# Kernel optimization log

Measured on AMD Instinct MI355X. Metric: run time of the kernel, lower is better.

Reference implementation:

```python
import jax, jax.numpy as jnp
import numpy as np
import math

B, S, E = 4, 4096, 1024
NUM_HEADS = 16
D = E // NUM_HEADS  # attention_size = 64


def setup_inputs() -> dict:
    key = jax.random.key(0)
    ks = jax.random.split(key, 7)
    queries = jax.random.normal(ks[0], (B, S, E), dtype=jnp.float32)
    keys = jax.random.normal(ks[1], (B, S, E), dtype=jnp.float32)
    values = jax.random.normal(ks[2], (B, S, E), dtype=jnp.float32)
    mask = jax.random.randint(ks[3], (B, S, S), 0, 2).astype(bool)
    # nn.Linear(E, D, bias=False): weight [D, E], y = x @ W^T
    lim = 1.0 / math.sqrt(E)
    W_q = jax.random.uniform(ks[4], (D, E), jnp.float32, -lim, lim)
    W_k = jax.random.uniform(ks[5], (D, E), jnp.float32, -lim, lim)
    W_v = jax.random.uniform(ks[6], (D, E), jnp.float32, -lim, lim)
    return {"queries": queries, "keys": keys, "values": values, "mask": mask,
            "W_q": W_q, "W_k": W_k, "W_v": W_v}


def reference(queries, keys, values, mask, W_q, W_k, W_v):
    Q = jnp.einsum('bse,de->bsd', queries, W_q)  # [B,S,D]
    K = jnp.einsum('bse,de->bsd', keys, W_k)
    V = jnp.einsum('bse,de->bsd', values, W_v)
    norm = math.sqrt(D)
    scores = jnp.einsum('bqd,bkd->bqk', Q, K) / norm  # [B,S,S]
    scores = jnp.where(mask, jnp.float32(-1e20), scores)
    attn = jax.nn.softmax(scores, axis=2)
    return jnp.einsum('bqk,bkd->bqd', attn, V)  # [B,S,D]
```

## Files before the change

kernel.cpp:

```cpp
#include <hip/hip_runtime.h>
#include <hip/hip_bf16.h>
#include <math.h>

#define NB 4
#define NS 4096
#define NE 1024
#define ND 64

typedef short bf16x8 __attribute__((ext_vector_type(8)));
typedef float f32x4  __attribute__((ext_vector_type(4)));

__device__ unsigned short g_Wb[3 * ND * NE];
__device__ unsigned short g_Qp[NB * NS * ND];
__device__ unsigned short g_Kp[NB * NS * ND];
__device__ unsigned short g_Vt[NB * ND * NS];
__device__ int g_flag;

static __device__ inline unsigned short f2bf(float f) {
    __hip_bfloat16 h = __float2bfloat16(f);
    return *reinterpret_cast<unsigned short*>(&h);
}
static __device__ inline unsigned int f2bf2(float lo, float hi) {
    __hip_bfloat162 h = __float22bfloat162_rn(make_float2(lo, hi));
    return *reinterpret_cast<unsigned int*>(&h);
}

static __device__ __forceinline__ void lds_fence() {
    asm volatile("s_waitcnt lgkmcnt(0)" ::: "memory");
}

__global__ void detect_mask(const unsigned int* __restrict__ mw) {
    __shared__ int found;
    if (threadIdx.x == 0) found = 0;
    __syncthreads();
    int f = 0;
    for (int i = threadIdx.x; i < 4096; i += 256)
        if (mw[i] > 1u) f = 1;
    if (f) atomicOr(&found, 1);
    __syncthreads();
    if (threadIdx.x == 0) g_flag = found;
}

__global__ void prep_w(const float* __restrict__ Wq, const float* __restrict__ Wk,
                       const float* __restrict__ Wv) {
    const int z = blockIdx.x;
    const float* W = (z == 0) ? Wq : (z == 1) ? Wk : Wv;
    unsigned short* o = g_Wb + (size_t)z * (ND * NE);
    const float scale = (z == 0) ? 0.125f : 1.0f;
    int i0 = blockIdx.y * 2048 + threadIdx.x * 8;
    float4 a = *(const float4*)&W[i0];
    float4 b = *(const float4*)&W[i0 + 4];
    ushort4 u0 = { f2bf(a.x * scale), f2bf(a.y * scale), f2bf(a.z * scale), f2bf(a.w * scale) };
    ushort4 u1 = { f2bf(b.x * scale), f2bf(b.y * scale), f2bf(b.z * scale), f2bf(b.w * scale) };
    *(ushort4*)&o[i0]     = u0;
    *(ushort4*)&o[i0 + 4] = u1;
}

__global__ __launch_bounds__(256) void proj_kernel(
    const float* __restrict__ Xq, const float* __restrict__ Xk, const float* __restrict__ Xv)
{
    __shared__ unsigned short Xs[2][64][72];

    const int z = blockIdx.y;
    const float* X = (z == 0) ? Xq : (z == 1) ? Xk : Xv;
    const unsigned short* W = g_Wb + (size_t)z * (ND * NE);

    const int t    = threadIdx.x;
    const int wv   = t >> 6;
    const int lane = t & 63;
    const int quad = lane >> 4;
    const int l16  = lane & 15;
    const int m0   = blockIdx.x * 64;

    const int sr  = t >> 4;
    const int sc4 = (t & 15) * 4;
    const float* Xb = X + (size_t)m0 * NE;

    float4 xr[4][4];

    #pragma unroll
    for (int d = 0; d < 4; ++d)
        #pragma unroll
        for (int p = 0; p < 4; ++p)
            xr[d][p] = *(const float4*)&Xb[(size_t)(sr + p * 16) * NE + d * 64 + sc4];
    #pragma unroll
    for (int p = 0; p < 4; ++p) {
        uint2 u = { f2bf2(xr[0][p].x, xr[0][p].y), f2bf2(xr[0][p].z, xr[0][p].w) };
        *(uint2*)&Xs[0][sr + p * 16][sc4] = u;
    }
    __syncthreads();

    f32x4 acc[4] = {};

    #pragma unroll
    for (int c = 0; c < 16; ++c) {
        if (c + 4 < 16) {
            #pragma unroll
            for (int p = 0; p < 4; ++p)
                xr[c & 3][p] = *(const float4*)&Xb[(size_t)(sr + p * 16) * NE + (c + 4) * 64 + sc4];
        }

        #pragma unroll
        for (int ks = 0; ks < 2; ++ks) {
            bf16x8 a = *(const bf16x8*)&Xs[c & 1][wv * 16 + l16][ks * 32 + quad * 8];
            #pragma unroll
            for (int nt = 0; nt < 4; ++nt) {
                bf16x8 bb = *(const bf16x8*)&W[(size_t)(nt * 16 + l16) * NE + c * 64 + ks * 32 + quad * 8];
                acc[nt] = __builtin_amdgcn_mfma_f32_16x16x32_bf16(a, bb, acc[nt], 0, 0, 0);
            }
        }

        if (c + 1 < 16) {
            #pragma unroll
            for (int p = 0; p < 4; ++p) {
                float4 v = xr[(c + 1) & 3][p];
                uint2 u = { f2bf2(v.x, v.y), f2bf2(v.z, v.w) };
                *(uint2*)&Xs[(c + 1) & 1][sr + p * 16][sc4] = u;
            }
        }
        __syncthreads();
    }

    #pragma unroll
    for (int nt = 0; nt < 4; ++nt)
        #pragma unroll
        for (int r = 0; r < 4; ++r) {
            int m   = m0 + wv * 16 + quad * 4 + r;
            int col = nt * 16 + l16;
            unsigned short u = f2bf(acc[nt][r]);
            if (z == 0)      g_Qp[(size_t)m * ND + col] = u;
            else if (z == 1) g_Kp[(size_t)m * ND + col] = u;
            else             g_Vt[((size_t)(m >> 12) * ND + col) * NS + (m & 4095)] = u;
        }
}

__global__ __launch_bounds__(256, 4) void attn_kernel(
    const void* __restrict__ maskp, float* __restrict__ out)
{
    __shared__ __align__(16) char smem[28672];
    short (*Ss)[2][16][72]         = reinterpret_cast<short(*)[2][16][72]>(smem);
    unsigned char (*Mb)[2][16][80] = reinterpret_cast<unsigned char(*)[2][16][80]>(smem + 18432);
    float (*Op)[16][68]            = reinterpret_cast<float(*)[16][68]>(smem);
    float (*Lp)[16]                = reinterpret_cast<float(*)[16]>(smem + 17408);

    const int t    = threadIdx.x;
    const int wv   = t >> 6;
    const int lane = t & 63;
    const int quad = lane >> 4;
    const int l16  = lane & 15;
    const int b    = blockIdx.y;
    const int q0   = blockIdx.x * 16;
    const int koff = wv * 1024;

    const bool m_u8 = (g_flag != 0);
    const unsigned char* m8  = (const unsigned char*)maskp;
    const int*           m32 = (const int*)maskp;

    const unsigned short* Qrow = g_Qp + ((size_t)b * NS + q0 + l16) * ND;
    const bf16x8 qf0 = *(const bf16x8*)&Qrow[quad * 8];
    const bf16x8 qf1 = *(const bf16x8*)&Qrow[32 + quad * 8];

    const unsigned short* Kbase = g_Kp + ((size_t)b * NS) * ND;
    const unsigned short* Vbase = g_Vt + (size_t)b * ND * NS;

    const int srow = lane >> 2;
    const int scol = (lane & 3) * 16;
    const unsigned char* m8row = m8 + ((size_t)b * NS + q0 + srow) * (size_t)NS + scol;

    if (m_u8) {
        uint4 mr0 = *(const uint4*)&m8row[koff];
        *(uint4*)&Mb[wv][0][srow][scol] = mr0;
    }

    float l_lane[4] = {};
    f32x4 Oacc[4] = {};

    #pragma unroll 2
    for (int it = 0; it < 16; ++it) {
        const int k0 = koff + it * 64;
        const int pb = it & 1;

        f32x4 sc[4] = {};
        #pragma unroll
        for (int kt = 0; kt < 4; ++kt) {
            const unsigned short* Krow = Kbase + (size_t)(k0 + kt * 16 + l16) * ND;
            bf16x8 kf0 = *(const bf16x8*)&Krow[quad * 8];
            bf16x8 kf1 = *(const bf16x8*)&Krow[32 + quad * 8];
            sc[kt] = __builtin_amdgcn_mfma_f32_16x16x32_bf16(qf0, kf0, sc[kt], 0, 0, 0);
            sc[kt] = __builtin_amdgcn_mfma_f32_16x16x32_bf16(qf1, kf1, sc[kt], 0, 0, 0);
        }

        uint4 mr = {};
        if (m_u8 && it < 15)
            mr = *(const uint4*)&m8row[k0 + 64];

        bf16x8 vf[8];
        #pragma unroll
        for (int nt = 0; nt < 4; ++nt) {
            const unsigned short* Vrow = Vbase + (size_t)(nt * 16 + l16) * NS + k0;
            vf[2 * nt]     = *(const bf16x8*)&Vrow[quad * 8];
            vf[2 * nt + 1] = *(const bf16x8*)&Vrow[32 + quad * 8];
        }

        int mvv[16];
        if (m_u8) {
            #pragma unroll
            for (int kt = 0; kt < 4; ++kt)
                #pragma unroll
                for (int r = 0; r < 4; ++r)
                    mvv[kt * 4 + r] = Mb[wv][pb][quad * 4 + r][kt * 16 + l16];
        } else {
            #pragma unroll
            for (int r = 0; r < 4; ++r) {
                size_t mrow = ((size_t)b * NS + (q0 + quad * 4 + r)) * (size_t)NS + k0;
                #pragma unroll
                for (int kt = 0; kt < 4; ++kt)
                    mvv[kt * 4 + r] = m32[mrow + kt * 16 + l16];
            }
        }

        #pragma unroll
        for (int kt = 0; kt < 4; ++kt)
            #pragma unroll
            for (int r = 0; r < 4; ++r) {
                float p = mvv[kt * 4 + r] ? 0.0f : __expf(sc[kt][r]);
                l_lane[r] += p;
                Ss[wv][pb][quad * 4 + r][kt * 16 + l16] = (short)f2bf(p);
            }

        if (m_u8 && it < 15)
            *(uint4*)&Mb[wv][pb ^ 1][srow][scol] = mr;

        lds_fence();

        bf16x8 a0 = *(const bf16x8*)&Ss[wv][pb][l16][quad * 8];
        bf16x8 a1 = *(const bf16x8*)&Ss[wv][pb][l16][32 + quad * 8];

        __builtin_amdgcn_s_setprio(1);
        #pragma unroll
        for (int nt = 0; nt < 4; ++nt) {
            Oacc[nt] = __builtin_amdgcn_mfma_f32_16x16x32_bf16(a0, vf[2 * nt],     Oacc[nt], 0, 0, 0);
            Oacc[nt] = __builtin_amdgcn_mfma_f32_16x16x32_bf16(a1, vf[2 * nt + 1], Oacc[nt], 0, 0, 0);
        }
        __builtin_amdgcn_s_setprio(0);
    }

    __syncthreads();

    #pragma unroll
    for (int r = 0; r < 4; ++r) {
        #pragma unroll
        for (int off = 1; off < 16; off <<= 1)
            l_lane[r] += __shfl_xor(l_lane[r], off);
    }

    #pragma unroll
    for (int nt = 0; nt < 4; ++nt)
        #pragma unroll
        for (int r = 0; r < 4; ++r)
            Op[wv][quad * 4 + r][nt * 16 + l16] = Oacc[nt][r];
    if (l16 == 0) {
        #pragma unroll
        for (int r = 0; r < 4; ++r)
            Lp[wv][quad * 4 + r] = l_lane[r];
    }
    __syncthreads();

    {
        int q  = t >> 4;
        int d4 = (t & 15) * 4;
        f32x4 s = {};
        #pragma unroll
        for (int w = 0; w < 4; ++w)
            s += *(const f32x4*)&Op[w][q][d4];
        float l = Lp[0][q] + Lp[1][q] + Lp[2][q] + Lp[3][q];
        float inv = 1.0f / l;
        float4 o = { s[0] * inv, s[1] * inv, s[2] * inv, s[3] * inv };
        *(float4*)&out[((size_t)b * NS + q0 + q) * ND + d4] = o;
    }
}

extern "C" void kernel_launch(void* const* d_in, const int* in_sizes, int n_in,
                              void* d_out, int out_size, void* d_ws, size_t ws_size,
                              hipStream_t stream) {
    const float* queries = (const float*)d_in[0];
    const float* keys    = (const float*)d_in[1];
    const float* values  = (const float*)d_in[2];
    const void*  mask    = d_in[3];
    const float* Wq      = (const float*)d_in[4];
    const float* Wk      = (const float*)d_in[5];
    const float* Wv      = (const float*)d_in[6];
    float* out = (float*)d_out;

    hipLaunchKernelGGL(detect_mask, dim3(1), dim3(256), 0, stream,
                       (const unsigned int*)mask);
    hipLaunchKernelGGL(prep_w, dim3(3, 32), dim3(256), 0, stream, Wq, Wk, Wv);
    hipLaunchKernelGGL(proj_kernel, dim3((NB * NS) / 64, 3), dim3(256), 0, stream,
                       queries, keys, values);
    hipLaunchKernelGGL(attn_kernel, dim3(NS / 16, NB), dim3(256), 0, stream,
                       mask, out);
}
```

Measured before the change: 607.2 us.

## Share K/V tiles in LDS across waves with async global-to-LDS double buffering

The attention kernel now gives each block 64 query rows (16 per wave) instead of splitting the key range across waves. K and V tiles are loaded once per block into swizzled, double-buffered LDS with global_load_lds, and the mask bytes are prefetched two tiles ahead. Masking is applied to the packed bf16 probability fragments, the row sum is taken from those fragments, and the cross-wave reduction of partial outputs is removed. Blocks are mapped so that each XCD works on a single batch for L2 locality. In exchange the kernel adds a block-wide barrier every tile and holds fewer blocks (a quarter as many).

```diff
diff --git a/kernel.cpp b/kernel.cpp
--- a/kernel.cpp
+++ b/kernel.cpp
@@ -24,9 +24,14 @@
     __hip_bfloat162 h = __float22bfloat162_rn(make_float2(lo, hi));
     return *reinterpret_cast<unsigned int*>(&h);
 }
-
-static __device__ __forceinline__ void lds_fence() {
-    asm volatile("s_waitcnt lgkmcnt(0)" ::: "memory");
+static __device__ inline float bf2f(short s) {
+    return __uint_as_float(((unsigned int)(unsigned short)s) << 16);
+}
+
+#define AS1 __attribute__((address_space(1)))
+#define AS3 __attribute__((address_space(3)))
+static __device__ __forceinline__ void gll16(const void* g, void* l) {
+    __builtin_amdgcn_global_load_lds((const AS1 void*)g, (AS3 void*)l, 16, 0, 0);
 }
 
 __global__ void detect_mask(const unsigned int* __restrict__ mw) {
@@ -134,149 +139,218 @@
         }
 }
 
-__global__ __launch_bounds__(256, 4) void attn_kernel(
+__global__ __launch_bounds__(256) void attn_kernel(
     const void* __restrict__ maskp, float* __restrict__ out)
 {
-    __shared__ __align__(16) char smem[28672];
-    short (*Ss)[2][16][72]         = reinterpret_cast<short(*)[2][16][72]>(smem);
-    unsigned char (*Mb)[2][16][80] = reinterpret_cast<unsigned char(*)[2][16][80]>(smem + 18432);
-    float (*Op)[16][68]            = reinterpret_cast<float(*)[16][68]>(smem);
-    float (*Lp)[16]                = reinterpret_cast<float(*)[16]>(smem + 17408);
+    __shared__ unsigned short KT[2][64 * 64];
+    __shared__ unsigned short VT[2][64 * 64];
+    __shared__ unsigned char  MR[4][4][1024];
+    __shared__ short          Ss[4][16][72];
 
     const int t    = threadIdx.x;
     const int wv   = t >> 6;
     const int lane = t & 63;
     const int quad = lane >> 4;
     const int l16  = lane & 15;
-    const int b    = blockIdx.y;
-    const int q0   = blockIdx.x * 16;
-    const int koff = wv * 1024;
+
+    const int n    = blockIdx.x;
+    const int xcd  = n & 7;
+    const int b    = xcd >> 1;
+    const int q0   = ((n >> 3) * 2 + (xcd & 1)) * 64;
+    const int wq0  = q0 + wv * 16;
 
     const bool m_u8 = (g_flag != 0);
     const unsigned char* m8  = (const unsigned char*)maskp;
     const int*           m32 = (const int*)maskp;
 
-    const unsigned short* Qrow = g_Qp + ((size_t)b * NS + q0 + l16) * ND;
+    const unsigned short* Qrow = g_Qp + ((size_t)b * NS + wq0 + l16) * ND;
     const bf16x8 qf0 = *(const bf16x8*)&Qrow[quad * 8];
     const bf16x8 qf1 = *(const bf16x8*)&Qrow[32 + quad * 8];
 
     const unsigned short* Kbase = g_Kp + ((size_t)b * NS) * ND;
     const unsigned short* Vbase = g_Vt + (size_t)b * ND * NS;
 
-    const int srow = lane >> 2;
-    const int scol = (lane & 3) * 16;
-    const unsigned char* m8row = m8 + ((size_t)b * NS + q0 + srow) * (size_t)NS + scol;
+    const int r8 = lane >> 3;
+    const int c8 = lane & 7;
+    const int sw = c8 ^ r8;
+
+    const unsigned char* m8base =
+        m8 + ((size_t)b * NS + wq0 + (lane >> 2)) * (size_t)NS + (lane & 3) * 16;
+
+    float l_row = 0.0f;
+    f32x4 Oacc[4] = {};
+
+    const int rsw = l16 & 7;
 
     if (m_u8) {
-        uint4 mr0 = *(const uint4*)&m8row[koff];
-        *(uint4*)&Mb[wv][0][srow][scol] = mr0;
+        #pragma unroll
+        for (int j = 0; j < 2; ++j) {
+            const int row = wv * 16 + j * 8 + r8;
+            gll16(Kbase + (size_t)row * 64 + sw * 8, &KT[0][(wv * 16 + j * 8) * 64]);
+            gll16(Vbase + (size_t)row * 4096 + sw * 8, &VT[0][(wv * 16 + j * 8) * 64]);
+        }
+        gll16(m8base, &MR[0][wv][0]);
+        gll16(m8base + 64, &MR[1][wv][0]);
+        asm volatile("s_waitcnt vmcnt(1)" ::: "memory");
+        __builtin_amdgcn_s_barrier();
+
+        #pragma unroll 2
+        for (int it = 0; it < 64; ++it) {
+            const int buf = it & 1;
+            const int k0  = it * 64;
+
+            if (it < 63) {
+                const int k1 = k0 + 64;
+                #pragma unroll
+                for (int j = 0; j < 2; ++j) {
+                    const int row = wv * 16 + j * 8 + r8;
+                    gll16(Kbase + (size_t)(k1 + row) * 64 + sw * 8,
+                          &KT[buf ^ 1][(wv * 16 + j * 8) * 64]);
+                    gll16(Vbase + (size_t)row * 4096 + k1 + sw * 8,
+                          &VT[buf ^ 1][(wv * 16 + j * 8) * 64]);
+                }
+            }
+            if (it < 62)
+                gll16(m8base + (it + 2) * 64, &MR[(it + 2) & 3][wv][0]);
+
+            f32x4 sc[4] = {};
+            #pragma unroll
+            for (int kt = 0; kt < 4; ++kt) {
+                const int row = kt * 16 + l16;
+                bf16x8 kf0 = *(const bf16x8*)&KT[buf][row * 64 + ((quad ^ rsw) << 3)];
+                bf16x8 kf1 = *(const bf16x8*)&KT[buf][row * 64 + (((4 + quad) ^ rsw) << 3)];
+                sc[kt] = __builtin_amdgcn_mfma_f32_16x16x32_bf16(qf0, kf0, sc[kt], 0, 0, 0);
+                sc[kt] = __builtin_amdgcn_mfma_f32_16x16x32_bf16(qf1, kf1, sc[kt], 0, 0, 0);
+            }
+
+            #pragma unroll
+            for (int kt = 0; kt < 4; ++kt)
+                #pragma unroll
+                for (int r = 0; r < 4; ++r)
+                    Ss[wv][quad * 4 + r][kt * 16 + l16] = (short)f2bf(__expf(sc[kt][r]));
+
+            asm volatile("s_waitcnt lgkmcnt(0)" ::: "memory");
+
+            bf16x8 a0 = *(const bf16x8*)&Ss[wv][l16][quad * 8];
+            bf16x8 a1 = *(const bf16x8*)&Ss[wv][l16][32 + quad * 8];
+            {
+                const unsigned char* MRt = &MR[it & 3][wv][0];
+                uint2 mm0 = *(const uint2*)&MRt[l16 * 64 + quad * 8];
+                uint2 mm1 = *(const uint2*)&MRt[l16 * 64 + 32 + quad * 8];
+                #pragma unroll
+                for (int j = 0; j < 4; ++j) {
+                    a0[j]     = ((mm0.x >> (8 * j)) & 255u) ? (short)0 : a0[j];
+                    a0[4 + j] = ((mm0.y >> (8 * j)) & 255u) ? (short)0 : a0[4 + j];
+                    a1[j]     = ((mm1.x >> (8 * j)) & 255u) ? (short)0 : a1[j];
+                    a1[4 + j] = ((mm1.y >> (8 * j)) & 255u) ? (short)0 : a1[4 + j];
+                }
+            }
+            {
+                float ls = 0.0f;
+                #pragma unroll
+                for (int j = 0; j < 8; ++j) ls += bf2f(a0[j]) + bf2f(a1[j]);
+                l_row += ls;
+            }
+            #pragma unroll
+            for (int nt = 0; nt < 4; ++nt) {
+                const int row = nt * 16 + l16;
+                bf16x8 vf0 = *(const bf16x8*)&VT[buf][row * 64 + ((quad ^ rsw) << 3)];
+                bf16x8 vf1 = *(const bf16x8*)&VT[buf][row * 64 + (((4 + quad) ^ rsw) << 3)];
+                Oacc[nt] = __builtin_amdgcn_mfma_f32_16x16x32_bf16(a0, vf0, Oacc[nt], 0, 0, 0);
+                Oacc[nt] = __builtin_amdgcn_mfma_f32_16x16x32_bf16(a1, vf1, Oacc[nt], 0, 0, 0);
+            }
+
+            if (it < 63) {
+                if (it < 62) asm volatile("s_waitcnt vmcnt(1)" ::: "memory");
+                else         asm volatile("s_waitcnt vmcnt(0)" ::: "memory");
+                __builtin_amdgcn_s_barrier();
+            }
+        }
+    } else {
+        #pragma unroll
+        for (int j = 0; j < 2; ++j) {
+            const int row = wv * 16 + j * 8 + r8;
+            gll16(Kbase + (size_t)row * 64 + sw * 8, &KT[0][(wv * 16 + j * 8) * 64]);
+            gll16(Vbase + (size_t)row * 4096 + sw * 8, &VT[0][(wv * 16 + j * 8) * 64]);
+        }
+        asm volatile("s_waitcnt vmcnt(0)" ::: "memory");
+        __builtin_amdgcn_s_barrier();
+
+        #pragma unroll 2
+        for (int it = 0; it < 64; ++it) {
+            const int buf = it & 1;
+            const int k0  = it * 64;
+
+            if (it < 63) {
+                const int k1 = k0 + 64;
+                #pragma unroll
+                for (int j = 0; j < 2; ++j) {
+                    const int row = wv * 16 + j * 8 + r8;
+                    gll16(Kbase + (size_t)(k1 + row) * 64 + sw * 8,
+                          &KT[buf ^ 1][(wv * 16 + j * 8) * 64]);
+                    gll16(Vbase + (size_t)row * 4096 + k1 + sw * 8,
+                          &VT[buf ^ 1][(wv * 16 + j * 8) * 64]);
+                }
+            }
+
+            f32x4 sc[4] = {};
+            #pragma unroll
+            for (int kt = 0; kt < 4; ++kt) {
+                const int row = kt * 16 + l16;
+                bf16x8 kf0 = *(const bf16x8*)&KT[buf][row * 64 + ((quad ^ rsw) << 3)];
+                bf16x8 kf1 = *(const bf16x8*)&KT[buf][row * 64 + (((4 + quad) ^ rsw) << 3)];
+                sc[kt] = __builtin_amdgcn_mfma_f32_16x16x32_bf16(qf0, kf0, sc[kt], 0, 0, 0);
+                sc[kt] = __builtin_amdgcn_mfma_f32_16x16x32_bf16(qf1, kf1, sc[kt], 0, 0, 0);
+            }
+
+            #pragma unroll
+            for (int r = 0; r < 4; ++r) {
+                size_t mrow = ((size_t)b * NS + (wq0 + quad * 4 + r)) * (size_t)NS + k0;
+                #pragma unroll
+                for (int kt = 0; kt < 4; ++kt) {
+                    int mv = m32[mrow + kt * 16 + l16];
+                    float p = mv ? 0.0f : __expf(sc[kt][r]);
+                    Ss[wv][quad * 4 + r][kt * 16 + l16] = (short)f2bf(p);
+                }
+            }
+
+            asm volatile("s_waitcnt lgkmcnt(0)" ::: "memory");
+
+            bf16x8 a0 = *(const bf16x8*)&Ss[wv][l16][quad * 8];
+            bf16x8 a1 = *(const bf16x8*)&Ss[wv][l16][32 + quad * 8];
+            {
+                float ls = 0.0f;
+                #pragma unroll
+                for (int j = 0; j < 8; ++j) ls += bf2f(a0[j]) + bf2f(a1[j]);
+                l_row += ls;
+            }
+            #pragma unroll
+            for (int nt = 0; nt < 4; ++nt) {
+                const int row = nt * 16 + l16;
+                bf16x8 vf0 = *(const bf16x8*)&VT[buf][row * 64 + ((quad ^ rsw) << 3)];
+                bf16x8 vf1 = *(const bf16x8*)&VT[buf][row * 64 + (((4 + quad) ^ rsw) << 3)];
+                Oacc[nt] = __builtin_amdgcn_mfma_f32_16x16x32_bf16(a0, vf0, Oacc[nt], 0, 0, 0);
+                Oacc[nt] = __builtin_amdgcn_mfma_f32_16x16x32_bf16(a1, vf1, Oacc[nt], 0, 0, 0);
+            }
+
+            if (it < 63) {
+                asm volatile("s_waitcnt vmcnt(0)" ::: "memory");
+                __builtin_amdgcn_s_barrier();
+            }
+        }
     }
 
-    float l_lane[4] = {};
-    f32x4 Oacc[4] = {};
-
-    #pragma unroll 2
-    for (int it = 0; it < 16; ++it) {
-        const int k0 = koff + it * 64;
-        const int pb = it & 1;
-
-        f32x4 sc[4] = {};
-        #pragma unroll
-        for (int kt = 0; kt < 4; ++kt) {
-            const unsigned short* Krow = Kbase + (size_t)(k0 + kt * 16 + l16) * ND;
-            bf16x8 kf0 = *(const bf16x8*)&Krow[quad * 8];
-            bf16x8 kf1 = *(const bf16x8*)&Krow[32 + quad * 8];
-            sc[kt] = __builtin_amdgcn_mfma_f32_16x16x32_bf16(qf0, kf0, sc[kt], 0, 0, 0);
-            sc[kt] = __builtin_amdgcn_mfma_f32_16x16x32_bf16(qf1, kf1, sc[kt], 0, 0, 0);
-        }
-
-        uint4 mr = {};
-        if (m_u8 && it < 15)
-            mr = *(const uint4*)&m8row[k0 + 64];
-
-        bf16x8 vf[8];
-        #pragma unroll
-        for (int nt = 0; nt < 4; ++nt) {
-            const unsigned short* Vrow = Vbase + (size_t)(nt * 16 + l16) * NS + k0;
-            vf[2 * nt]     = *(const bf16x8*)&Vrow[quad * 8];
-            vf[2 * nt + 1] = *(const bf16x8*)&Vrow[32 + quad * 8];
-        }
-
-        int mvv[16];
-        if (m_u8) {
-            #pragma unroll
-            for (int kt = 0; kt < 4; ++kt)
-                #pragma unroll
-                for (int r = 0; r < 4; ++r)
-                    mvv[kt * 4 + r] = Mb[wv][pb][quad * 4 + r][kt * 16 + l16];
-        } else {
-            #pragma unroll
-            for (int r = 0; r < 4; ++r) {
-                size_t mrow = ((size_t)b * NS + (q0 + quad * 4 + r)) * (size_t)NS + k0;
-                #pragma unroll
-                for (int kt = 0; kt < 4; ++kt)
-                    mvv[kt * 4 + r] = m32[mrow + kt * 16 + l16];
-            }
-        }
-
-        #pragma unroll
-        for (int kt = 0; kt < 4; ++kt)
-            #pragma unroll
-            for (int r = 0; r < 4; ++r) {
-                float p = mvv[kt * 4 + r] ? 0.0f : __expf(sc[kt][r]);
-                l_lane[r] += p;
-                Ss[wv][pb][quad * 4 + r][kt * 16 + l16] = (short)f2bf(p);
-            }
-
-        if (m_u8 && it < 15)
-            *(uint4*)&Mb[wv][pb ^ 1][srow][scol] = mr;
-
-        lds_fence();
-
-        bf16x8 a0 = *(const bf16x8*)&Ss[wv][pb][l16][quad * 8];
-        bf16x8 a1 = *(const bf16x8*)&Ss[wv][pb][l16][32 + quad * 8];
-
-        __builtin_amdgcn_s_setprio(1);
-        #pragma unroll
-        for (int nt = 0; nt < 4; ++nt) {
-            Oacc[nt] = __builtin_amdgcn_mfma_f32_16x16x32_bf16(a0, vf[2 * nt],     Oacc[nt], 0, 0, 0);
-            Oacc[nt] = __builtin_amdgcn_mfma_f32_16x16x32_bf16(a1, vf[2 * nt + 1], Oacc[nt], 0, 0, 0);
-        }
-        __builtin_amdgcn_s_setprio(0);
-    }
-
-    __syncthreads();
+    l_row += __shfl_xor(l_row, 16);
+    l_row += __shfl_xor(l_row, 32);
+    const float inv = 1.0f / l_row;
 
     #pragma unroll
     for (int r = 0; r < 4; ++r) {
-        #pragma unroll
-        for (int off = 1; off < 16; off <<= 1)
-            l_lane[r] += __shfl_xor(l_lane[r], off);
-    }
-
-    #pragma unroll
-    for (int nt = 0; nt < 4; ++nt)
-        #pragma unroll
-        for (int r = 0; r < 4; ++r)
-            Op[wv][quad * 4 + r][nt * 16 + l16] = Oacc[nt][r];
-    if (l16 == 0) {
-        #pragma unroll
-        for (int r = 0; r < 4; ++r)
-            Lp[wv][quad * 4 + r] = l_lane[r];
-    }
-    __syncthreads();
-
-    {
-        int q  = t >> 4;
-        int d4 = (t & 15) * 4;
-        f32x4 s = {};
-        #pragma unroll
-        for (int w = 0; w < 4; ++w)
-            s += *(const f32x4*)&Op[w][q][d4];
-        float l = Lp[0][q] + Lp[1][q] + Lp[2][q] + Lp[3][q];
-        float inv = 1.0f / l;
-        float4 o = { s[0] * inv, s[1] * inv, s[2] * inv, s[3] * inv };
-        *(float4*)&out[((size_t)b * NS + q0 + q) * ND + d4] = o;
+        const float invm = __shfl(inv, quad * 4 + r);
+        const int m = wq0 + quad * 4 + r;
+        #pragma unroll
+        for (int nt = 0; nt < 4; ++nt)
+            out[((size_t)b * NS + m) * ND + nt * 16 + l16] = Oacc[nt][r] * invm;
     }
 }
 
@@ -297,6 +371,6 @@
     hipLaunchKernelGGL(prep_w, dim3(3, 32), dim3(256), 0, stream, Wq, Wk, Wv);
     hipLaunchKernelGGL(proj_kernel, dim3((NB * NS) / 64, 3), dim3(256), 0, stream,
                        queries, keys, values);
-    hipLaunchKernelGGL(attn_kernel, dim3(NS / 16, NB), dim3(256), 0, stream,
+    hipLaunchKernelGGL(attn_kernel, dim3(NS / 64 * NB), dim3(256), 0, stream,
                        mask, out);
 }
```

Result: faster. 583.3 us (-3.9%).
